# Kernel optimization log

Measured on AMD Instinct MI355X. Metric: run time of the kernel, lower is better.

## Reference

```python
import jax, jax.numpy as jnp
import numpy as np

B, S, D, H = 4, 4096, 256, 4
Dh = D // H


def setup_inputs() -> dict:
    key = jax.random.key(0)
    ks = jax.random.split(key, 5)
    scale = 1.0 / np.sqrt(D)
    return {
        "inputs": jax.random.normal(ks[0], (B, S, D), dtype=jnp.float32),
        "Wq": jax.random.normal(ks[1], (D, D), dtype=jnp.float32) * scale,
        "bq": jnp.zeros((D,), jnp.float32),
        "Wk": jax.random.normal(ks[2], (D, D), dtype=jnp.float32) * scale,
        "bk": jnp.zeros((D,), jnp.float32),
        "Wv": jax.random.normal(ks[3], (D, D), dtype=jnp.float32) * scale,
        "bv": jnp.zeros((D,), jnp.float32),
        "Wo": jax.random.normal(ks[4], (D, D), dtype=jnp.float32) * scale,
        "bo": jnp.zeros((D,), jnp.float32),
    }


def reference(inputs, Wq, bq, Wk, bk, Wv, bv, Wo, bo):
    b, s, d = inputs.shape
    # QKV projections
    q = inputs @ Wq + bq
    k = inputs @ Wk + bk
    v = inputs @ Wv + bv
    # separate heads: [B, S, D] -> [B, H, S, Dh]
    def split_heads(x):
        return x.reshape(b, s, H, Dh).transpose(0, 2, 1, 3)
    q, k, v = split_heads(q), split_heads(k), split_heads(v)
    # scaled dot-product attention (no causal mask: mask=False)
    scores = jnp.einsum("bhqd,bhkd->bhqk", q, k) / jnp.sqrt(jnp.float32(Dh))
    weights = jax.nn.softmax(scores, axis=-1)
    attn = jnp.einsum("bhqk,bhkd->bhqd", weights, v)
    # combine heads: [B, H, S, Dh] -> [B, S, D]
    attn = attn.transpose(0, 2, 1, 3).reshape(b, s, d)
    return attn @ Wo + bo
```

## Files before the change

### kernel.cpp

```cpp
#include <hip/hip_runtime.h>
#include <cmath>

#define B_  4
#define S_  4096
#define D_  256
#define H_  4
#define DH_ 64
#define M_TOTAL (B_*S_)
#define QSCALE 0.1803368801111f

typedef __bf16 bf16x8 __attribute__((ext_vector_type(8)));
typedef __bf16 bf16x4 __attribute__((ext_vector_type(4)));
typedef __bf16 bf16x2 __attribute__((ext_vector_type(2)));
typedef float  f32x4  __attribute__((ext_vector_type(4)));
typedef float  f32x16 __attribute__((ext_vector_type(16)));

#define AS1 __attribute__((address_space(1)))
#define AS3 __attribute__((address_space(3)))

__device__ __forceinline__ void g2lds16(const void* g, void* l) {
    __builtin_amdgcn_global_load_lds((AS1 const void*)g, (AS3 void*)l, 16, 0, 0);
}

#if __has_builtin(__builtin_amdgcn_permlane32_swap)
typedef unsigned uint2v __attribute__((ext_vector_type(2)));
__device__ __forceinline__ void plswap(unsigned &a, unsigned &b) {
    uint2v r = __builtin_amdgcn_permlane32_swap(a, b, false, false);
    a = r[0]; b = r[1];
}
#else
__device__ __forceinline__ void plswap(unsigned &a, unsigned &b) {
    unsigned bl = (unsigned)__shfl_xor((int)b, 32);
    unsigned ah = (unsigned)__shfl_xor((int)a, 32);
    bool hi = (threadIdx.x & 32) != 0;
    unsigned na = hi ? bl : a;
    unsigned nb = hi ? b  : ah;
    a = na; b = nb;
}
#endif

__device__ __forceinline__ unsigned pk2(float x, float y) {
    bf16x2 t; t[0] = (__bf16)x; t[1] = (__bf16)y;
    return __builtin_bit_cast(unsigned, t);
}

__global__ __launch_bounds__(256) void prep(const float* __restrict__ X,
                                            const float* __restrict__ W0,
                                            const float* __restrict__ W1,
                                            const float* __restrict__ W2,
                                            const float* __restrict__ W3,
                                            __bf16* __restrict__ Xb,
                                            __bf16* __restrict__ Wt_all) {
    int t = threadIdx.x;
    if (blockIdx.x < 2048) {
        size_t i = ((size_t)blockIdx.x * 256 + t) * 8;
        float4 v0 = *(const float4*)(X + i);
        float4 v1 = *(const float4*)(X + i + 4);
        bf16x8 o;
        o[0] = (__bf16)v0.x; o[1] = (__bf16)v0.y; o[2] = (__bf16)v0.z; o[3] = (__bf16)v0.w;
        o[4] = (__bf16)v1.x; o[5] = (__bf16)v1.y; o[6] = (__bf16)v1.z; o[7] = (__bf16)v1.w;
        *(bf16x8*)(Xb + i) = o;
        return;
    }
    int bid = blockIdx.x - 2048;
    int z = bid >> 6, rem = bid & 63;
    int by = rem >> 3, bx = rem & 7;
    const float* W = (z == 0) ? W0 : (z == 1) ? W1 : (z == 2) ? W2 : W3;
    float wsc = (z == 0) ? QSCALE : 1.0f;
    __bf16* Wt = Wt_all + (size_t)z * 65536;
    __shared__ float tile[32][33];
    int r0 = by * 32, c0 = bx * 32;
#pragma unroll
    for (int e = 0; e < 4; e++) {
        int idx = t + e * 256; int r = idx >> 5, c = idx & 31;
        tile[r][c] = W[(r0 + r) * 256 + c0 + c];
    }
    __syncthreads();
#pragma unroll
    for (int e = 0; e < 4; e++) {
        int idx = t + e * 256; int r = idx >> 5, c = idx & 31;
        Wt[(c0 + r) * 256 + (r0 + c)] = (__bf16)(tile[c][r] * wsc);
    }
}

__global__ __launch_bounds__(256) void gemm_bt(const __bf16* __restrict__ A,
                                               const __bf16* __restrict__ Wt_all,
                                               const float* __restrict__ bias0,
                                               const float* __restrict__ bias1,
                                               const float* __restrict__ bias2,
                                               __bf16* __restrict__ outb,
                                               __bf16* __restrict__ voutb,
                                               float* __restrict__ outf,
                                               int out_is_f32, float bsc0) {
    constexpr int K = 256;
    __shared__ __attribute__((aligned(16))) __bf16 As[128 * 32];
    __shared__ __attribute__((aligned(16))) __bf16 Bs[128 * 32];

    int t = threadIdx.x;
    int lane = t & 63, w = t >> 6;
    int wr = w >> 1, wc = w & 1;
    int l16 = lane & 15, quad = lane >> 4;
    int mbase = blockIdx.x * 128;
    int nbase = blockIdx.y * 128;
    int z = blockIdx.z;
    const __bf16* Bt = Wt_all + (size_t)z * 65536;
    const float* bias = (z == 0) ? bias0 : (z == 1) ? bias1 : bias2;
    float bscale = (z == 0) ? bsc0 : 1.0f;

    f32x4 acc[4][4] = {};

    int srow = t >> 2;
    int sseg = (t & 3) * 8;

    for (int kk = 0; kk < K; kk += 32) {
        __syncthreads();
        g2lds16(A  + (size_t)(mbase +      srow) * K + kk + sseg, (char*)As +        t * 16);
        g2lds16(A  + (size_t)(mbase + 64 + srow) * K + kk + sseg, (char*)As + 4096 + t * 16);
        g2lds16(Bt + (size_t)(nbase +      srow) * K + kk + sseg, (char*)Bs +        t * 16);
        g2lds16(Bt + (size_t)(nbase + 64 + srow) * K + kk + sseg, (char*)Bs + 4096 + t * 16);
        __syncthreads();

        bf16x8 a[4], b[4];
#pragma unroll
        for (int i = 0; i < 4; i++)
            a[i] = *(const bf16x8*)(As + (wr * 64 + i * 16 + l16) * 32 + quad * 8);
#pragma unroll
        for (int j = 0; j < 4; j++)
            b[j] = *(const bf16x8*)(Bs + (wc * 64 + j * 16 + l16) * 32 + quad * 8);
#pragma unroll
        for (int i = 0; i < 4; i++)
#pragma unroll
            for (int j = 0; j < 4; j++)
                acc[i][j] = __builtin_amdgcn_mfma_f32_16x16x32_bf16(a[i], b[j], acc[i][j], 0, 0, 0);
    }

#pragma unroll
    for (int i = 0; i < 4; i++) {
#pragma unroll
        for (int j = 0; j < 4; j++) {
            int col = nbase + wc * 64 + j * 16 + l16;
            float bv = bias[col] * bscale;
            int row0 = mbase + wr * 64 + i * 16 + quad * 4;
            if (out_is_f32) {
#pragma unroll
                for (int r = 0; r < 4; r++)
                    outf[(size_t)(row0 + r) * 256 + col] = acc[i][j][r] + bv;
            } else if (z == 2) {
                int hcol = col >> 6, dh = col & 63;
                int bidx = row0 >> 12, s0 = row0 & 4095;
                bf16x4 pk;
#pragma unroll
                for (int r = 0; r < 4; r++) pk[r] = (__bf16)(acc[i][j][r] + bv);
                *(bf16x4*)(voutb + ((size_t)(bidx * 4 + hcol) * 64 + dh) * 4096 + s0) = pk;
            } else {
#pragma unroll
                for (int r = 0; r < 4; r++)
                    outb[(size_t)z * ((size_t)M_TOTAL * 256) + (size_t)(row0 + r) * 256 + col] =
                        (__bf16)(acc[i][j][r] + bv);
            }
        }
    }
}

__global__ __launch_bounds__(64) void attn(const __bf16* __restrict__ Qb,
                                           const __bf16* __restrict__ Kb,
                                           const __bf16* __restrict__ Vt,
                                           __bf16* __restrict__ Ctx) {
    __shared__ __attribute__((aligned(16))) __bf16 smem[16384];

    int lane = threadIdx.x & 63;
    int l31 = lane & 31, hh = lane >> 5;

    int lin = blockIdx.x;
    int xcd = lin & 7, j = lin >> 3;
    int bh = xcd * 2 + (j & 1);
    int qblk = j >> 1;
    int b = bh >> 2, hd = bh & 3;
    int qw = qblk * 64;

    const __bf16* Kbase = Kb + (size_t)b * S_ * 256 + hd * 64;
    const __bf16* Vbase = Vt + (size_t)bh * 64 * S_;

    bf16x8 qf[4][2];
#pragma unroll
    for (int ks = 0; ks < 4; ks++)
#pragma unroll
        for (int qt = 0; qt < 2; qt++)
            qf[ks][qt] = *(const bf16x8*)(Qb + (size_t)(b * S_ + qw + qt * 32 + l31) * 256
                                              + hd * 64 + ks * 16 + hh * 8);

    f32x16 acc[2][2] = {};
    float lsum[2] = {0.f, 0.f};

    int srow = lane >> 3;
    int sseg = lane & 7;

#define STAGE(kv, buf) do {                                                    \
        char* mk = (char*)smem + (buf) * 16384;                                \
        char* mv = mk + 8192;                                                  \
        _Pragma("unroll")                                                      \
        for (int c = 0; c < 8; c++) {                                          \
            int rr = c * 8 + srow;                                             \
            int gseg = (sseg ^ (rr & 7)) * 8;                                  \
            g2lds16(Kbase + (size_t)((kv) + rr) * 256 + gseg,                  \
                    mk + c * 1024 + lane * 16);                                \
            g2lds16(Vbase + (size_t)rr * S_ + (kv) + gseg,                     \
                    mv + c * 1024 + lane * 16);                                \
        }                                                                      \
    } while (0)

    STAGE(0, 0);

    for (int it = 0; it < 64; it++) {
        int buf = it & 1;
        if (it < 63) {
            STAGE((it + 1) * 64, buf ^ 1);
            asm volatile("s_waitcnt vmcnt(16)" ::: "memory");
        } else {
            asm volatile("s_waitcnt vmcnt(0)" ::: "memory");
        }
        __bf16* Ksp = (__bf16*)((char*)smem + buf * 16384);
        __bf16* Vsp = (__bf16*)((char*)smem + buf * 16384 + 8192);

        f32x16 st[2][2] = {};
#pragma unroll
        for (int kt = 0; kt < 2; kt++) {
            bf16x8 kf[4];
#pragma unroll
            for (int ks = 0; ks < 4; ks++) {
                int slot = (ks * 2 + hh) ^ (l31 & 7);
                kf[ks] = *(const bf16x8*)(Ksp + (kt * 32 + l31) * 64 + slot * 8);
            }
#pragma unroll
            for (int ks = 0; ks < 4; ks++)
#pragma unroll
                for (int qt = 0; qt < 2; qt++)
                    st[kt][qt] = __builtin_amdgcn_mfma_f32_32x32x16_bf16(kf[ks], qf[ks][qt], st[kt][qt], 0, 0, 0);
        }

#pragma unroll
        for (int kt = 0; kt < 2; kt++) {
            unsigned dd[2][8];
#pragma unroll
            for (int qt = 0; qt < 2; qt++) {
                float p[16];
#pragma unroll
                for (int r = 0; r < 16; r++) p[r] = __builtin_amdgcn_exp2f(st[kt][qt][r]);
                float s0 = ((p[0] + p[1]) + (p[2] + p[3])) + ((p[4] + p[5]) + (p[6] + p[7]));
                float s1 = ((p[8] + p[9]) + (p[10] + p[11])) + ((p[12] + p[13]) + (p[14] + p[15]));
                lsum[qt] += s0 + s1;
#pragma unroll
                for (int m = 0; m < 4; m++) {
                    dd[qt][m * 2]     = pk2(p[4 * m],     p[4 * m + 1]);
                    dd[qt][m * 2 + 1] = pk2(p[4 * m + 2], p[4 * m + 3]);
                }
            }
#pragma unroll
            for (int tt = 0; tt < 2; tt++) {
                int tks = kt * 2 + tt;
                bf16x8 pf[2];
#pragma unroll
                for (int qt = 0; qt < 2; qt++) {
                    unsigned x0 = dd[qt][4 * tt],     y0 = dd[qt][4 * tt + 2];
                    unsigned x1 = dd[qt][4 * tt + 1], y1 = dd[qt][4 * tt + 3];
                    plswap(x0, y0);
                    plswap(x1, y1);
                    union { unsigned u[4]; bf16x8 v; } c;
                    c.u[0] = x0; c.u[1] = x1; c.u[2] = y0; c.u[3] = y1;
                    pf[qt] = c.v;
                }
#pragma unroll
                for (int mt = 0; mt < 2; mt++) {
                    int slot = (tks * 2 + hh) ^ (l31 & 7);
                    bf16x8 vf = *(const bf16x8*)(Vsp + (mt * 32 + l31) * 64 + slot * 8);
#pragma unroll
                    for (int qt = 0; qt < 2; qt++)
                        acc[mt][qt] = __builtin_amdgcn_mfma_f32_32x32x16_bf16(vf, pf[qt], acc[mt][qt], 0, 0, 0);
                }
            }
        }
    }
#undef STAGE

    float inv[2];
#pragma unroll
    for (int qt = 0; qt < 2; qt++) {
        float l = lsum[qt];
        l += __shfl_xor(l, 32);
        inv[qt] = 1.f / l;
    }

    __bf16* Es = smem;
#pragma unroll
    for (int qt = 0; qt < 2; qt++)
#pragma unroll
        for (int mt = 0; mt < 2; mt++)
#pragma unroll
            for (int rg = 0; rg < 4; rg++) {
                bf16x4 ov;
#pragma unroll
                for (int e = 0; e < 4; e++)
                    ov[e] = (__bf16)(acc[mt][qt][4 * rg + e] * inv[qt]);
                int dhb = mt * 32 + rg * 8 + 4 * hh;
                *(bf16x4*)(Es + (qt * 32 + l31) * 72 + dhb) = ov;
            }
#pragma unroll
    for (int pass = 0; pass < 8; pass++) {
        int q = pass * 8 + (lane >> 3);
        int col = (lane & 7) * 8;
        bf16x8 val = *(const bf16x8*)(Es + q * 72 + col);
        *(bf16x8*)(Ctx + (size_t)(b * S_ + qw + q) * 256 + hd * 64 + col) = val;
    }
}

extern "C" void kernel_launch(void* const* d_in, const int* in_sizes, int n_in,
                              void* d_out, int out_size, void* d_ws, size_t ws_size,
                              hipStream_t stream) {
    const float* X  = (const float*)d_in[0];
    const float* Wq = (const float*)d_in[1];
    const float* bq = (const float*)d_in[2];
    const float* Wk = (const float*)d_in[3];
    const float* bk = (const float*)d_in[4];
    const float* Wv = (const float*)d_in[5];
    const float* bv = (const float*)d_in[6];
    const float* Wo = (const float*)d_in[7];
    const float* bo = (const float*)d_in[8];
    float* out = (float*)d_out;

    char* ws = (char*)d_ws;
    const size_t MB = 1024 * 1024;
    __bf16* Xb  = (__bf16*)(ws);
    __bf16* Ctx = (__bf16*)(ws);
    __bf16* Wt  = (__bf16*)(ws + 8 * MB);
    __bf16* Qb  = (__bf16*)(ws + 8 * MB + 512 * 1024);
    __bf16* Kb  = (__bf16*)((char*)Qb + 8 * MB);
    __bf16* Vt  = (__bf16*)((char*)Kb + 8 * MB);

    prep<<<dim3(2304), dim3(256), 0, stream>>>(X, Wq, Wk, Wv, Wo, Xb, Wt);
    gemm_bt<<<dim3(M_TOTAL / 128, 2, 3), dim3(256), 0, stream>>>(
        Xb, Wt, bq, bk, bv, Qb, Vt, nullptr, 0, QSCALE);
    attn<<<dim3(1024), dim3(64), 0, stream>>>(Qb, Kb, Vt, Ctx);
    gemm_bt<<<dim3(M_TOTAL / 128, 2, 1), dim3(256), 0, stream>>>(
        Ctx, Wt + 3 * 65536, bo, bo, bo, nullptr, nullptr, out, 1, 1.0f);
}
```

Baseline: 201.2 us.

## Share K/V tiles across four waves per attention block with 4-slot ring

The attention kernel moves from one 64-query wave per block to 256-thread blocks of four waves, each handling 32 queries. All four waves share K/V tiles staged cooperatively into LDS, so global K/V traffic per query drops. The double buffer becomes a 4-slot ring with prefetch distance 2, and a workgroup barrier is added each iteration. In exchange, each wave gets half the per-fragment MFMA reuse, pays per-iteration barriers, and uses 64KB of LDS per block, while the smaller per-wave working set allows more resident waves per CU.

```diff
diff --git a/kernel.cpp b/kernel.cpp
--- a/kernel.cpp
+++ b/kernel.cpp
@@ -162,13 +162,14 @@
     }
 }
 
-__global__ __launch_bounds__(64) void attn(const __bf16* __restrict__ Qb,
-                                           const __bf16* __restrict__ Kb,
-                                           const __bf16* __restrict__ Vt,
-                                           __bf16* __restrict__ Ctx) {
-    __shared__ __attribute__((aligned(16))) __bf16 smem[16384];
-
-    int lane = threadIdx.x & 63;
+__global__ __launch_bounds__(256, 2) void attn(const __bf16* __restrict__ Qb,
+                                               const __bf16* __restrict__ Kb,
+                                               const __bf16* __restrict__ Vt,
+                                               __bf16* __restrict__ Ctx) {
+    __shared__ __attribute__((aligned(16))) __bf16 smem[32768];
+
+    int t = threadIdx.x;
+    int lane = t & 63, w = t >> 6;
     int l31 = lane & 31, hh = lane >> 5;
 
     int lin = blockIdx.x;
@@ -176,53 +177,55 @@
     int bh = xcd * 2 + (j & 1);
     int qblk = j >> 1;
     int b = bh >> 2, hd = bh & 3;
-    int qw = qblk * 64;
+    int qw = qblk * 128 + w * 32;
 
     const __bf16* Kbase = Kb + (size_t)b * S_ * 256 + hd * 64;
     const __bf16* Vbase = Vt + (size_t)bh * 64 * S_;
 
-    bf16x8 qf[4][2];
+    bf16x8 qf[4];
 #pragma unroll
     for (int ks = 0; ks < 4; ks++)
-#pragma unroll
-        for (int qt = 0; qt < 2; qt++)
-            qf[ks][qt] = *(const bf16x8*)(Qb + (size_t)(b * S_ + qw + qt * 32 + l31) * 256
-                                              + hd * 64 + ks * 16 + hh * 8);
-
-    f32x16 acc[2][2] = {};
-    float lsum[2] = {0.f, 0.f};
-
-    int srow = lane >> 3;
-    int sseg = lane & 7;
-
-#define STAGE(kv, buf) do {                                                    \
-        char* mk = (char*)smem + (buf) * 16384;                                \
+        qf[ks] = *(const bf16x8*)(Qb + (size_t)(b * S_ + qw + l31) * 256
+                                      + hd * 64 + ks * 16 + hh * 8);
+
+    f32x16 acc[2] = {};
+    float lsum = 0.f;
+
+    int srow = t >> 3;
+    int sseg = t & 7;
+
+#define STAGE(kv, slot) do {                                                   \
+        char* mk = (char*)smem + (slot) * 16384;                               \
         char* mv = mk + 8192;                                                  \
         _Pragma("unroll")                                                      \
-        for (int c = 0; c < 8; c++) {                                          \
-            int rr = c * 8 + srow;                                             \
+        for (int c = 0; c < 2; c++) {                                          \
+            int rr = c * 32 + srow;                                            \
             int gseg = (sseg ^ (rr & 7)) * 8;                                  \
             g2lds16(Kbase + (size_t)((kv) + rr) * 256 + gseg,                  \
-                    mk + c * 1024 + lane * 16);                                \
+                    mk + c * 4096 + t * 16);                                   \
             g2lds16(Vbase + (size_t)rr * S_ + (kv) + gseg,                     \
-                    mv + c * 1024 + lane * 16);                                \
+                    mv + c * 4096 + t * 16);                                   \
         }                                                                      \
     } while (0)
 
     STAGE(0, 0);
+    STAGE(64, 1);
 
     for (int it = 0; it < 64; it++) {
-        int buf = it & 1;
-        if (it < 63) {
-            STAGE((it + 1) * 64, buf ^ 1);
-            asm volatile("s_waitcnt vmcnt(16)" ::: "memory");
+        if (it < 62) {
+            STAGE((it + 2) * 64, (it + 2) & 3);
+            asm volatile("s_waitcnt vmcnt(8)" ::: "memory");
+        } else if (it == 62) {
+            asm volatile("s_waitcnt vmcnt(4)" ::: "memory");
         } else {
             asm volatile("s_waitcnt vmcnt(0)" ::: "memory");
         }
-        __bf16* Ksp = (__bf16*)((char*)smem + buf * 16384);
-        __bf16* Vsp = (__bf16*)((char*)smem + buf * 16384 + 8192);
-
-        f32x16 st[2][2] = {};
+        asm volatile("s_barrier" ::: "memory");
+
+        __bf16* Ksp = (__bf16*)((char*)smem + (it & 3) * 16384);
+        __bf16* Vsp = Ksp + 4096;
+
+        f32x16 st[2] = {};
 #pragma unroll
         for (int kt = 0; kt < 2; kt++) {
             bf16x8 kf[4];
@@ -233,79 +236,63 @@
             }
 #pragma unroll
             for (int ks = 0; ks < 4; ks++)
-#pragma unroll
-                for (int qt = 0; qt < 2; qt++)
-                    st[kt][qt] = __builtin_amdgcn_mfma_f32_32x32x16_bf16(kf[ks], qf[ks][qt], st[kt][qt], 0, 0, 0);
+                st[kt] = __builtin_amdgcn_mfma_f32_32x32x16_bf16(kf[ks], qf[ks], st[kt], 0, 0, 0);
         }
 
 #pragma unroll
         for (int kt = 0; kt < 2; kt++) {
-            unsigned dd[2][8];
-#pragma unroll
-            for (int qt = 0; qt < 2; qt++) {
-                float p[16];
-#pragma unroll
-                for (int r = 0; r < 16; r++) p[r] = __builtin_amdgcn_exp2f(st[kt][qt][r]);
-                float s0 = ((p[0] + p[1]) + (p[2] + p[3])) + ((p[4] + p[5]) + (p[6] + p[7]));
-                float s1 = ((p[8] + p[9]) + (p[10] + p[11])) + ((p[12] + p[13]) + (p[14] + p[15]));
-                lsum[qt] += s0 + s1;
-#pragma unroll
-                for (int m = 0; m < 4; m++) {
-                    dd[qt][m * 2]     = pk2(p[4 * m],     p[4 * m + 1]);
-                    dd[qt][m * 2 + 1] = pk2(p[4 * m + 2], p[4 * m + 3]);
-                }
+            float p[16];
+#pragma unroll
+            for (int r = 0; r < 16; r++) p[r] = __builtin_amdgcn_exp2f(st[kt][r]);
+            float s0 = ((p[0] + p[1]) + (p[2] + p[3])) + ((p[4] + p[5]) + (p[6] + p[7]));
+            float s1 = ((p[8] + p[9]) + (p[10] + p[11])) + ((p[12] + p[13]) + (p[14] + p[15]));
+            lsum += s0 + s1;
+            unsigned dd[8];
+#pragma unroll
+            for (int m = 0; m < 4; m++) {
+                dd[m * 2]     = pk2(p[4 * m],     p[4 * m + 1]);
+                dd[m * 2 + 1] = pk2(p[4 * m + 2], p[4 * m + 3]);
             }
 #pragma unroll
             for (int tt = 0; tt < 2; tt++) {
                 int tks = kt * 2 + tt;
-                bf16x8 pf[2];
-#pragma unroll
-                for (int qt = 0; qt < 2; qt++) {
-                    unsigned x0 = dd[qt][4 * tt],     y0 = dd[qt][4 * tt + 2];
-                    unsigned x1 = dd[qt][4 * tt + 1], y1 = dd[qt][4 * tt + 3];
-                    plswap(x0, y0);
-                    plswap(x1, y1);
-                    union { unsigned u[4]; bf16x8 v; } c;
-                    c.u[0] = x0; c.u[1] = x1; c.u[2] = y0; c.u[3] = y1;
-                    pf[qt] = c.v;
-                }
+                unsigned x0 = dd[4 * tt],     y0 = dd[4 * tt + 2];
+                unsigned x1 = dd[4 * tt + 1], y1 = dd[4 * tt + 3];
+                plswap(x0, y0);
+                plswap(x1, y1);
+                union { unsigned u[4]; bf16x8 v; } c;
+                c.u[0] = x0; c.u[1] = x1; c.u[2] = y0; c.u[3] = y1;
 #pragma unroll
                 for (int mt = 0; mt < 2; mt++) {
                     int slot = (tks * 2 + hh) ^ (l31 & 7);
                     bf16x8 vf = *(const bf16x8*)(Vsp + (mt * 32 + l31) * 64 + slot * 8);
-#pragma unroll
-                    for (int qt = 0; qt < 2; qt++)
-                        acc[mt][qt] = __builtin_amdgcn_mfma_f32_32x32x16_bf16(vf, pf[qt], acc[mt][qt], 0, 0, 0);
+                    acc[mt] = __builtin_amdgcn_mfma_f32_32x32x16_bf16(vf, c.v, acc[mt], 0, 0, 0);
                 }
             }
         }
     }
 #undef STAGE
 
-    float inv[2];
-#pragma unroll
-    for (int qt = 0; qt < 2; qt++) {
-        float l = lsum[qt];
-        l += __shfl_xor(l, 32);
-        inv[qt] = 1.f / l;
-    }
-
-    __bf16* Es = smem;
-#pragma unroll
-    for (int qt = 0; qt < 2; qt++)
-#pragma unroll
-        for (int mt = 0; mt < 2; mt++)
-#pragma unroll
-            for (int rg = 0; rg < 4; rg++) {
-                bf16x4 ov;
-#pragma unroll
-                for (int e = 0; e < 4; e++)
-                    ov[e] = (__bf16)(acc[mt][qt][4 * rg + e] * inv[qt]);
-                int dhb = mt * 32 + rg * 8 + 4 * hh;
-                *(bf16x4*)(Es + (qt * 32 + l31) * 72 + dhb) = ov;
-            }
-#pragma unroll
-    for (int pass = 0; pass < 8; pass++) {
+    float l = lsum;
+    l += __shfl_xor(l, 32);
+    float inv = 1.f / l;
+
+    __syncthreads();
+    __bf16* Es = smem + w * 2304;
+#pragma unroll
+    for (int mt = 0; mt < 2; mt++) {
+#pragma unroll
+        for (int rg = 0; rg < 4; rg++) {
+            bf16x4 ov;
+#pragma unroll
+            for (int e = 0; e < 4; e++) ov[e] = (__bf16)(acc[mt][4 * rg + e] * inv);
+            int dhb = mt * 32 + rg * 8 + 4 * hh;
+            *(bf16x4*)(Es + l31 * 72 + dhb) = ov;
+        }
+    }
+    __syncthreads();
+#pragma unroll
+    for (int pass = 0; pass < 4; pass++) {
         int q = pass * 8 + (lane >> 3);
         int col = (lane & 7) * 8;
         bf16x8 val = *(const bf16x8*)(Es + q * 72 + col);
@@ -339,7 +326,7 @@
     prep<<<dim3(2304), dim3(256), 0, stream>>>(X, Wq, Wk, Wv, Wo, Xb, Wt);
     gemm_bt<<<dim3(M_TOTAL / 128, 2, 3), dim3(256), 0, stream>>>(
         Xb, Wt, bq, bk, bv, Qb, Vt, nullptr, 0, QSCALE);
-    attn<<<dim3(1024), dim3(64), 0, stream>>>(Qb, Kb, Vt, Ctx);
+    attn<<<dim3(512), dim3(256), 0, stream>>>(Qb, Kb, Vt, Ctx);
     gemm_bt<<<dim3(M_TOTAL / 128, 2, 1), dim3(256), 0, stream>>>(
         Ctx, Wt + 3 * 65536, bo, bo, bo, nullptr, nullptr, out, 1, 1.0f);
 }
```

Result: faster. 181.6 us (-9.7%).

## Share K/V tiles across four waves with split-KV and four-stage LDS ring

Applied to the files above, without the earlier changes.

The attention kernel changes from one wave per block to four waves per block. Two waves cover 128 query rows between them, and each half of a wave pair processes half of every 64-key tile. Every staged K/V tile is now consumed by two query groups, which halves global and L2 traffic for K and V. The LDS pipeline becomes a 4-slot ring prefetching two tiles ahead, with a workgroup barrier every iteration. At the end, partial accumulators and row sums from the two key halves are reduced through LDS before normalization and writeback. In exchange it adds per-iteration barrier sync and a 64KB LDS footprint that limits how many blocks fit per CU.

```diff
diff --git a/kernel.cpp b/kernel.cpp
--- a/kernel.cpp
+++ b/kernel.cpp
@@ -162,21 +162,23 @@
     }
 }
 
-__global__ __launch_bounds__(64) void attn(const __bf16* __restrict__ Qb,
-                                           const __bf16* __restrict__ Kb,
-                                           const __bf16* __restrict__ Vt,
-                                           __bf16* __restrict__ Ctx) {
-    __shared__ __attribute__((aligned(16))) __bf16 smem[16384];
-
-    int lane = threadIdx.x & 63;
+__global__ __launch_bounds__(256, 2) void attn(const __bf16* __restrict__ Qb,
+                                               const __bf16* __restrict__ Kb,
+                                               const __bf16* __restrict__ Vt,
+                                               __bf16* __restrict__ Ctx) {
+    __shared__ __attribute__((aligned(16))) __bf16 smem[32768];
+
+    int t = threadIdx.x;
+    int lane = t & 63, w = t >> 6;
     int l31 = lane & 31, hh = lane >> 5;
+    int kw = w & 1, qw2 = w >> 1;
 
     int lin = blockIdx.x;
     int xcd = lin & 7, j = lin >> 3;
     int bh = xcd * 2 + (j & 1);
     int qblk = j >> 1;
     int b = bh >> 2, hd = bh & 3;
-    int qw = qblk * 64;
+    int qw = qblk * 128 + qw2 * 64;
 
     const __bf16* Kbase = Kb + (size_t)b * S_ * 256 + hd * 64;
     const __bf16* Vbase = Vt + (size_t)bh * 64 * S_;
@@ -192,124 +194,156 @@
     f32x16 acc[2][2] = {};
     float lsum[2] = {0.f, 0.f};
 
-    int srow = lane >> 3;
-    int sseg = lane & 7;
-
-#define STAGE(kv, buf) do {                                                    \
-        char* mk = (char*)smem + (buf) * 16384;                                \
+    int srow = t >> 3;
+    int sseg = t & 7;
+
+#define STAGE(kv, slot) do {                                                   \
+        char* mk = (char*)smem + (slot) * 16384;                               \
         char* mv = mk + 8192;                                                  \
         _Pragma("unroll")                                                      \
-        for (int c = 0; c < 8; c++) {                                          \
-            int rr = c * 8 + srow;                                             \
+        for (int c = 0; c < 2; c++) {                                          \
+            int rr = c * 32 + srow;                                            \
             int gseg = (sseg ^ (rr & 7)) * 8;                                  \
             g2lds16(Kbase + (size_t)((kv) + rr) * 256 + gseg,                  \
-                    mk + c * 1024 + lane * 16);                                \
+                    mk + c * 4096 + t * 16);                                   \
             g2lds16(Vbase + (size_t)rr * S_ + (kv) + gseg,                     \
-                    mv + c * 1024 + lane * 16);                                \
+                    mv + c * 4096 + t * 16);                                   \
         }                                                                      \
     } while (0)
 
     STAGE(0, 0);
+    STAGE(64, 1);
 
     for (int it = 0; it < 64; it++) {
-        int buf = it & 1;
-        if (it < 63) {
-            STAGE((it + 1) * 64, buf ^ 1);
-            asm volatile("s_waitcnt vmcnt(16)" ::: "memory");
+        if (it < 62) {
+            STAGE((it + 2) * 64, (it + 2) & 3);
+            asm volatile("s_waitcnt vmcnt(8)" ::: "memory");
+        } else if (it == 62) {
+            asm volatile("s_waitcnt vmcnt(4)" ::: "memory");
         } else {
             asm volatile("s_waitcnt vmcnt(0)" ::: "memory");
         }
-        __bf16* Ksp = (__bf16*)((char*)smem + buf * 16384);
-        __bf16* Vsp = (__bf16*)((char*)smem + buf * 16384 + 8192);
-
-        f32x16 st[2][2] = {};
-#pragma unroll
-        for (int kt = 0; kt < 2; kt++) {
-            bf16x8 kf[4];
-#pragma unroll
-            for (int ks = 0; ks < 4; ks++) {
-                int slot = (ks * 2 + hh) ^ (l31 & 7);
-                kf[ks] = *(const bf16x8*)(Ksp + (kt * 32 + l31) * 64 + slot * 8);
+        asm volatile("s_barrier" ::: "memory");
+
+        __bf16* Ksp = (__bf16*)((char*)smem + (it & 3) * 16384);
+        __bf16* Vsp = Ksp + 4096;
+
+        bf16x8 kf[4];
+#pragma unroll
+        for (int ks = 0; ks < 4; ks++) {
+            int slot = (ks * 2 + hh) ^ (l31 & 7);
+            kf[ks] = *(const bf16x8*)(Ksp + (kw * 32 + l31) * 64 + slot * 8);
+        }
+        f32x16 st[2] = {};
+#pragma unroll
+        for (int ks = 0; ks < 4; ks++)
+#pragma unroll
+            for (int qt = 0; qt < 2; qt++)
+                st[qt] = __builtin_amdgcn_mfma_f32_32x32x16_bf16(kf[ks], qf[ks][qt], st[qt], 0, 0, 0);
+
+        unsigned dd[2][8];
+#pragma unroll
+        for (int qt = 0; qt < 2; qt++) {
+            float p[16];
+#pragma unroll
+            for (int r = 0; r < 16; r++) p[r] = __builtin_amdgcn_exp2f(st[qt][r]);
+            float s0 = ((p[0] + p[1]) + (p[2] + p[3])) + ((p[4] + p[5]) + (p[6] + p[7]));
+            float s1 = ((p[8] + p[9]) + (p[10] + p[11])) + ((p[12] + p[13]) + (p[14] + p[15]));
+            lsum[qt] += s0 + s1;
+#pragma unroll
+            for (int m = 0; m < 4; m++) {
+                dd[qt][m * 2]     = pk2(p[4 * m],     p[4 * m + 1]);
+                dd[qt][m * 2 + 1] = pk2(p[4 * m + 2], p[4 * m + 3]);
             }
-#pragma unroll
-            for (int ks = 0; ks < 4; ks++)
+        }
+
+#pragma unroll
+        for (int tt = 0; tt < 2; tt++) {
+            int tks = kw * 2 + tt;
+            bf16x8 pf[2];
+#pragma unroll
+            for (int qt = 0; qt < 2; qt++) {
+                unsigned x0 = dd[qt][4 * tt],     y0 = dd[qt][4 * tt + 2];
+                unsigned x1 = dd[qt][4 * tt + 1], y1 = dd[qt][4 * tt + 3];
+                plswap(x0, y0);
+                plswap(x1, y1);
+                union { unsigned u[4]; bf16x8 v; } c;
+                c.u[0] = x0; c.u[1] = x1; c.u[2] = y0; c.u[3] = y1;
+                pf[qt] = c.v;
+            }
+#pragma unroll
+            for (int mt = 0; mt < 2; mt++) {
+                int slot = (tks * 2 + hh) ^ (l31 & 7);
+                bf16x8 vf = *(const bf16x8*)(Vsp + (mt * 32 + l31) * 64 + slot * 8);
 #pragma unroll
                 for (int qt = 0; qt < 2; qt++)
-                    st[kt][qt] = __builtin_amdgcn_mfma_f32_32x32x16_bf16(kf[ks], qf[ks][qt], st[kt][qt], 0, 0, 0);
-        }
-
-#pragma unroll
-        for (int kt = 0; kt < 2; kt++) {
-            unsigned dd[2][8];
-#pragma unroll
-            for (int qt = 0; qt < 2; qt++) {
-                float p[16];
-#pragma unroll
-                for (int r = 0; r < 16; r++) p[r] = __builtin_amdgcn_exp2f(st[kt][qt][r]);
-                float s0 = ((p[0] + p[1]) + (p[2] + p[3])) + ((p[4] + p[5]) + (p[6] + p[7]));
-                float s1 = ((p[8] + p[9]) + (p[10] + p[11])) + ((p[12] + p[13]) + (p[14] + p[15]));
-                lsum[qt] += s0 + s1;
-#pragma unroll
-                for (int m = 0; m < 4; m++) {
-                    dd[qt][m * 2]     = pk2(p[4 * m],     p[4 * m + 1]);
-                    dd[qt][m * 2 + 1] = pk2(p[4 * m + 2], p[4 * m + 3]);
+                    acc[mt][qt] = __builtin_amdgcn_mfma_f32_32x32x16_bf16(vf, pf[qt], acc[mt][qt], 0, 0, 0);
+            }
+        }
+    }
+#undef STAGE
+
+#pragma unroll
+    for (int qt = 0; qt < 2; qt++)
+        lsum[qt] += __shfl_xor(lsum[qt], 32);
+
+    __syncthreads();
+    float* lsd = (float*)((char*)smem + 32768);
+    if (kw == 1) {
+#pragma unroll
+        for (int mt = 0; mt < 2; mt++)
+#pragma unroll
+            for (int qt = 0; qt < 2; qt++)
+#pragma unroll
+                for (int g = 0; g < 4; g++) {
+                    f32x4 v;
+#pragma unroll
+                    for (int e = 0; e < 4; e++) v[e] = acc[mt][qt][4 * g + e];
+                    *(f32x4*)((char*)smem + qw2 * 16384
+                              + ((mt * 2 + qt) * 4 + g) * 1024 + lane * 16) = v;
                 }
-            }
-#pragma unroll
-            for (int tt = 0; tt < 2; tt++) {
-                int tks = kt * 2 + tt;
-                bf16x8 pf[2];
-#pragma unroll
-                for (int qt = 0; qt < 2; qt++) {
-                    unsigned x0 = dd[qt][4 * tt],     y0 = dd[qt][4 * tt + 2];
-                    unsigned x1 = dd[qt][4 * tt + 1], y1 = dd[qt][4 * tt + 3];
-                    plswap(x0, y0);
-                    plswap(x1, y1);
-                    union { unsigned u[4]; bf16x8 v; } c;
-                    c.u[0] = x0; c.u[1] = x1; c.u[2] = y0; c.u[3] = y1;
-                    pf[qt] = c.v;
+        lsd[qw2 * 128 + lane * 2 + 0] = lsum[0];
+        lsd[qw2 * 128 + lane * 2 + 1] = lsum[1];
+    }
+    __syncthreads();
+    if (kw == 0) {
+        float inv[2];
+#pragma unroll
+        for (int qt = 0; qt < 2; qt++)
+            inv[qt] = 1.f / (lsum[qt] + lsd[qw2 * 128 + lane * 2 + qt]);
+#pragma unroll
+        for (int mt = 0; mt < 2; mt++)
+#pragma unroll
+            for (int qt = 0; qt < 2; qt++)
+#pragma unroll
+                for (int g = 0; g < 4; g++) {
+                    f32x4 v = *(const f32x4*)((char*)smem + qw2 * 16384
+                                              + ((mt * 2 + qt) * 4 + g) * 1024 + lane * 16);
+#pragma unroll
+                    for (int e = 0; e < 4; e++) acc[mt][qt][4 * g + e] += v[e];
                 }
-#pragma unroll
-                for (int mt = 0; mt < 2; mt++) {
-                    int slot = (tks * 2 + hh) ^ (l31 & 7);
-                    bf16x8 vf = *(const bf16x8*)(Vsp + (mt * 32 + l31) * 64 + slot * 8);
-#pragma unroll
-                    for (int qt = 0; qt < 2; qt++)
-                        acc[mt][qt] = __builtin_amdgcn_mfma_f32_32x32x16_bf16(vf, pf[qt], acc[mt][qt], 0, 0, 0);
+
+        __bf16* Es = smem + 18432 + qw2 * 4608;
+#pragma unroll
+        for (int qt = 0; qt < 2; qt++)
+#pragma unroll
+            for (int mt = 0; mt < 2; mt++)
+#pragma unroll
+                for (int rg = 0; rg < 4; rg++) {
+                    bf16x4 ov;
+#pragma unroll
+                    for (int e = 0; e < 4; e++)
+                        ov[e] = (__bf16)(acc[mt][qt][4 * rg + e] * inv[qt]);
+                    int dhb = mt * 32 + rg * 8 + 4 * hh;
+                    *(bf16x4*)(Es + (qt * 32 + l31) * 72 + dhb) = ov;
                 }
-            }
-        }
-    }
-#undef STAGE
-
-    float inv[2];
-#pragma unroll
-    for (int qt = 0; qt < 2; qt++) {
-        float l = lsum[qt];
-        l += __shfl_xor(l, 32);
-        inv[qt] = 1.f / l;
-    }
-
-    __bf16* Es = smem;
-#pragma unroll
-    for (int qt = 0; qt < 2; qt++)
-#pragma unroll
-        for (int mt = 0; mt < 2; mt++)
-#pragma unroll
-            for (int rg = 0; rg < 4; rg++) {
-                bf16x4 ov;
-#pragma unroll
-                for (int e = 0; e < 4; e++)
-                    ov[e] = (__bf16)(acc[mt][qt][4 * rg + e] * inv[qt]);
-                int dhb = mt * 32 + rg * 8 + 4 * hh;
-                *(bf16x4*)(Es + (qt * 32 + l31) * 72 + dhb) = ov;
-            }
-#pragma unroll
-    for (int pass = 0; pass < 8; pass++) {
-        int q = pass * 8 + (lane >> 3);
-        int col = (lane & 7) * 8;
-        bf16x8 val = *(const bf16x8*)(Es + q * 72 + col);
-        *(bf16x8*)(Ctx + (size_t)(b * S_ + qw + q) * 256 + hd * 64 + col) = val;
+#pragma unroll
+        for (int pass = 0; pass < 8; pass++) {
+            int q = pass * 8 + (lane >> 3);
+            int col = (lane & 7) * 8;
+            bf16x8 val = *(const bf16x8*)(Es + q * 72 + col);
+            *(bf16x8*)(Ctx + (size_t)(b * S_ + qw + q) * 256 + hd * 64 + col) = val;
+        }
     }
 }
 
@@ -339,7 +373,7 @@
     prep<<<dim3(2304), dim3(256), 0, stream>>>(X, Wq, Wk, Wv, Wo, Xb, Wt);
     gemm_bt<<<dim3(M_TOTAL / 128, 2, 3), dim3(256), 0, stream>>>(
         Xb, Wt, bq, bk, bv, Qb, Vt, nullptr, 0, QSCALE);
-    attn<<<dim3(1024), dim3(64), 0, stream>>>(Qb, Kb, Vt, Ctx);
+    attn<<<dim3(512), dim3(256), 0, stream>>>(Qb, Kb, Vt, Ctx);
     gemm_bt<<<dim3(M_TOTAL / 128, 2, 1), dim3(256), 0, stream>>>(
         Ctx, Wt + 3 * 65536, bo, bo, bo, nullptr, nullptr, out, 1, 1.0f);
 }
```

After: 179.7 us. -10.7%, faster.
